# Kernel optimization log

Hardware: AMD Instinct MI355X
Metric: run time of the kernel (lower is better)

Reference implementation:

```python
import jax, jax.numpy as jnp
import numpy as np

TOP_K = 2
NUM_EXPERTS = 8

def setup_inputs() -> dict:
    key = jax.random.key(0)
    k_x, k_r, k_g, k_u, k_d = jax.random.split(key, 5)
    B, L, D, H, E = 1, 2048, 1024, 2048, NUM_EXPERTS
    scale = 0.02  # keep router logits / activations in a sane range
    return {
        "x": jax.random.normal(k_x, (B, L, D), dtype=jnp.float32),
        "router_w": jax.random.normal(k_r, (D, E), dtype=jnp.float32) * scale,
        "gate_w": jax.random.normal(k_g, (E, D, H), dtype=jnp.float32) * scale,
        "up_w": jax.random.normal(k_u, (E, D, H), dtype=jnp.float32) * scale,
        "down_w": jax.random.normal(k_d, (E, H, D), dtype=jnp.float32) * scale,
    }

def reference(x, router_w, gate_w, up_w, down_w):
    # x: (B, L, D)
    B, L, D = x.shape
    T = B * L
    E = router_w.shape[1]
    xf = x.reshape(T, D)

    # --- router: top-k softmax over selected logits (Mixtral-style) ---
    logits = xf @ router_w                      # (T, E)
    top_vals, top_idx = jax.lax.top_k(logits, TOP_K)  # (T, K)
    top_w = jax.nn.softmax(top_vals, axis=-1)   # (T, K)

    # combine weights scattered to dense (T, E); zeros for unrouted experts
    combine = jnp.zeros((T, E), dtype=x.dtype).at[
        jnp.arange(T)[:, None], top_idx
    ].add(top_w)

    # --- experts: SwiGLU, computed per expert, zero-weight tokens masked by combine ---
    gate = jnp.einsum('td,edh->eth', xf, gate_w)   # (E, T, H)
    up = jnp.einsum('td,edh->eth', xf, up_w)       # (E, T, H)
    hidden = jax.nn.silu(gate) * up                # (E, T, H)
    expert_out = jnp.einsum('eth,ehd->etd', hidden, down_w)  # (E, T, D)

    # --- weighted combine (equivalent to scatter_add over sorted assignments) ---
    y = jnp.einsum('etd,te->td', expert_out, combine)  # (T, D)
    return y.reshape(B, L, D)
```

## Files before the change

### kernel.cpp

```cpp
#include <hip/hip_runtime.h>
#include <hip/hip_bf16.h>
#include <stdint.h>

#define T_TOK 2048
#define DIM   1024
#define HDIM  2048
#define NE    8
#define ROWS_PAD 4224
#define TSLOTS 40

typedef __attribute__((ext_vector_type(8))) short bf16x8;
typedef __attribute__((ext_vector_type(8))) unsigned short u16x8;
typedef __attribute__((ext_vector_type(4))) float f32x4;

__device__ __forceinline__ unsigned short f2bf(float f) {
    union { float f; unsigned int u; } v; v.f = f;
    unsigned int r = v.u + 0x7FFF + ((v.u >> 16) & 1);
    return (unsigned short)(r >> 16);
}

__device__ __forceinline__ float bf2f(unsigned short b) {
    union { unsigned int u; float f; } v; v.u = ((unsigned int)b) << 16;
    return v.f;
}

__device__ __forceinline__ void gload16(const void* g, void* l) {
    __builtin_amdgcn_global_load_lds(
        (const __attribute__((address_space(1))) void*)g,
        (__attribute__((address_space(3))) void*)l, 16, 0, 0);
}

#define NTT 12288
__global__ void prep_kernel(const float* __restrict__ gw, const float* __restrict__ uw,
                            const float* __restrict__ dw,
                            unsigned short* __restrict__ WgT, unsigned short* __restrict__ WuT,
                            unsigned short* __restrict__ WdT,
                            const float* __restrict__ x, const float* __restrict__ rw,
                            int* __restrict__ counts, int* __restrict__ top_idx,
                            float* __restrict__ top_w) {
    __shared__ __align__(16) unsigned short lt[64 * 66];
    const int b = blockIdx.x;
    if (b < NTT) {
        const int m = b >> 12;
        const int t = b & 4095;
        const int e = t >> 9;
        const int rem = t & 511;
        const float* in; unsigned short* out; int R, C, by, bx;
        if (m == 0)      { in = gw; out = WgT; R = DIM;  C = HDIM; by = rem >> 5; bx = rem & 31; }
        else if (m == 1) { in = uw; out = WuT; R = DIM;  C = HDIM; by = rem >> 5; bx = rem & 31; }
        else             { in = dw; out = WdT; R = HDIM; C = DIM;  by = rem >> 4; bx = rem & 15; }
        const float* ip = in + (size_t)e * R * C + (size_t)(by * 64) * C + bx * 64;
        unsigned short* op = out + (size_t)e * R * C + (size_t)(bx * 64) * R + by * 64;
        const int r = threadIdx.x >> 2, g = threadIdx.x & 3;
#pragma unroll
        for (int i = 0; i < 4; ++i) {
            int s = g + 4 * i;
            float4 v = *(const float4*)&ip[(size_t)r * C + s * 4];
            ushort4 h;
            h.x = f2bf(v.x); h.y = f2bf(v.y); h.z = f2bf(v.z); h.w = f2bf(v.w);
            *(ushort4*)&lt[r * 66 + s * 4] = h;
        }
        __syncthreads();
        const int oc = threadIdx.x >> 2;
#pragma unroll
        for (int i = 0; i < 2; ++i) {
            int s = g + 4 * i;
            u16x8 h;
#pragma unroll
            for (int k = 0; k < 8; ++k)
                h[k] = lt[(s * 8 + k) * 66 + oc];
            *(u16x8*)&op[(size_t)oc * R + s * 8] = h;
        }
    } else {
        const int wid = (b - NTT) * 4 + (threadIdx.x >> 6);
        const int lane = threadIdx.x & 63;
        if (wid >= T_TOK) return;
        float acc[NE];
#pragma unroll
        for (int e = 0; e < NE; ++e) acc[e] = 0.f;
        const float* xr = x + (size_t)wid * DIM;
        for (int i = lane; i < DIM; i += 64) {
            float xv = xr[i];
            const float* wr = rw + (size_t)i * NE;
#pragma unroll
            for (int e = 0; e < NE; ++e) acc[e] += xv * wr[e];
        }
#pragma unroll
        for (int off = 32; off; off >>= 1) {
#pragma unroll
            for (int e = 0; e < NE; ++e) acc[e] += __shfl_xor(acc[e], off, 64);
        }
        if (lane == 0) {
            float v0 = -1e30f, v1 = -1e30f; int i0 = 0, i1 = 0;
#pragma unroll
            for (int e = 0; e < NE; ++e) {
                float v = acc[e];
                if (v > v0) { v1 = v0; i1 = i0; v0 = v; i0 = e; }
                else if (v > v1) { v1 = v; i1 = e; }
            }
            float e1 = __expf(v1 - v0);
            float s = 1.f + e1;
            top_idx[wid * 2]     = i0;
            top_idx[wid * 2 + 1] = i1;
            top_w[wid * 2]     = 1.f / s;
            top_w[wid * 2 + 1] = e1 / s;
            atomicAdd(&counts[i0], 1);
            atomicAdd(&counts[i1], 1);
        }
    }
}

__global__ void scan_kernel(const int* __restrict__ counts, int* __restrict__ offsets,
                            int* __restrict__ cursors,
                            int* __restrict__ tl_e, int* __restrict__ tl_m) {
    if (threadIdx.x == 0) {
        int run = 0;
        for (int e = 0; e < NE; ++e) { offsets[e] = run; cursors[e] = run; run += counts[e]; }
        int n = 0;
        for (int e = 0; e < NE; ++e) {
            int mt = (counts[e] + 127) >> 7;
            for (int m = 0; m < mt && n < 64; ++m) { tl_e[n] = e; tl_m[n] = m; ++n; }
        }
        for (; n < 64; ++n) tl_e[n] = -1;
    }
}

__global__ void gather_kernel(const float* __restrict__ x, const int* __restrict__ top_idx,
                              const float* __restrict__ top_w, int* __restrict__ cursors,
                              int* __restrict__ row_tok, float* __restrict__ row_w,
                              unsigned short* __restrict__ Abuf) {
    int t = blockIdx.x;
    __shared__ int pos[2];
    if (threadIdx.x < 2) {
        int k = threadIdx.x;
        int e = top_idx[t * 2 + k];
        int p = atomicAdd(&cursors[e], 1);
        pos[k] = p;
        row_tok[p] = t;
        row_w[p] = top_w[t * 2 + k];
    }
    __syncthreads();
    const float4* xr = (const float4*)(x + (size_t)t * DIM);
    float4 v = xr[threadIdx.x];
    ushort4 b;
    b.x = f2bf(v.x); b.y = f2bf(v.y); b.z = f2bf(v.z); b.w = f2bf(v.w);
    ushort4* A4 = (ushort4*)Abuf;
    A4[(size_t)pos[0] * (DIM / 4) + threadIdx.x] = b;
    A4[(size_t)pos[1] * (DIM / 4) + threadIdx.x] = b;
}

__global__ __launch_bounds__(256, 2)
void gemm1_kernel(const unsigned short* __restrict__ Abuf,
                  const unsigned short* __restrict__ WgT,
                  const unsigned short* __restrict__ WuT,
                  unsigned short* __restrict__ Hbuf,
                  const int* __restrict__ offsets, const int* __restrict__ counts,
                  const int* __restrict__ tl_e, const int* __restrict__ tl_m) {
    const int slot = blockIdx.y;
    const int e = tl_e[slot];
    if (e < 0) return;
    const int mtile = tl_m[slot];
    const int cnt = counts[e];
    const int n0 = blockIdx.x * 64;
    const int row0 = offsets[e] + mtile * 128;

    __shared__ __align__(16) unsigned char lds_raw[65536];
    unsigned short* AsB = (unsigned short*)lds_raw;
    unsigned short* BgB = (unsigned short*)(lds_raw + 32768);
    unsigned short* BuB = (unsigned short*)(lds_raw + 49152);
    unsigned short* ex  = (unsigned short*)lds_raw;

    const int tid = threadIdx.x;
    const int lane = tid & 63;
    const int wave = tid >> 6;
    const int wm = wave >> 1;
    const int wu = wave & 1;

    f32x4 acc[4][4];
#pragma unroll
    for (int i = 0; i < 4; ++i)
#pragma unroll
        for (int j = 0; j < 4; ++j) acc[i][j] = (f32x4){0.f, 0.f, 0.f, 0.f};

    const int srow = tid >> 3;
    const int sc0 = tid & 7;
    const unsigned short* Aab = Abuf + (size_t)row0 * DIM;
    const unsigned short* Bgb = WgT + (size_t)e * HDIM * DIM + (size_t)n0 * DIM;
    const unsigned short* Bub = WuT + (size_t)e * HDIM * DIM + (size_t)n0 * DIM;

    auto stage = [&](int buf, int kt) {
#pragma unroll
        for (int i = 0; i < 4; ++i) {
            int row = i * 32 + srow;
            int csrc = sc0 ^ (row & 7);
            gload16(Aab + (size_t)row * DIM + kt + csrc * 8,
                    AsB + buf * 8192 + (i * 256 + tid) * 8);
        }
#pragma unroll
        for (int i = 0; i < 2; ++i) {
            int row = i * 32 + srow;
            int csrc = sc0 ^ (row & 7);
            size_t go = (size_t)row * DIM + kt + csrc * 8;
            gload16(Bgb + go, BgB + buf * 4096 + (i * 256 + tid) * 8);
            gload16(Bub + go, BuB + buf * 4096 + (i * 256 + tid) * 8);
        }
    };

    const int rsel = lane & 15;
    const int csrcf = lane >> 4;

    stage(0, 0);
    int cur = 0;
    for (int kt = 0; kt < DIM; kt += 64) {
        __syncthreads();
        if (kt + 64 < DIM) stage(cur ^ 1, kt + 64);
        const unsigned short* Ac = AsB + cur * 8192;
        const unsigned short* Bc = (wu ? BuB : BgB) + cur * 4096;
#pragma unroll
        for (int kk = 0; kk < 2; ++kk) {
            bf16x8 af[4], bb[4];
#pragma unroll
            for (int i = 0; i < 4; ++i) {
                int ra = wm * 64 + i * 16 + rsel;
                af[i] = *(const bf16x8*)&Ac[ra * 64 + ((kk * 4 + csrcf) ^ (ra & 7)) * 8];
                int rb = i * 16 + rsel;
                bb[i] = *(const bf16x8*)&Bc[rb * 64 + ((kk * 4 + csrcf) ^ (rb & 7)) * 8];
            }
#pragma unroll
            for (int i = 0; i < 4; ++i)
#pragma unroll
                for (int j = 0; j < 4; ++j)
                    acc[i][j] = __builtin_amdgcn_mfma_f32_16x16x32_bf16(af[i], bb[j], acc[i][j], 0, 0, 0);
        }
        cur ^= 1;
    }

    const int c = lane & 15, rbase = (lane >> 4) * 4;
    const int obase = offsets[e];
    __syncthreads();
    if (wu) {
#pragma unroll
        for (int i = 0; i < 4; ++i)
#pragma unroll
            for (int r = 0; r < 4; ++r) {
                int row64 = i * 16 + rbase + r;
#pragma unroll
                for (int j = 0; j < 4; ++j)
                    ex[wm * 4096 + row64 * 64 + j * 16 + c] = f2bf(acc[i][j][r]);
            }
    }
    __syncthreads();
    if (!wu) {
#pragma unroll
        for (int i = 0; i < 4; ++i) {
#pragma unroll
            for (int r = 0; r < 4; ++r) {
                int row64 = i * 16 + rbase + r;
                int lrow = mtile * 128 + wm * 64 + row64;
                if (lrow < cnt) {
                    size_t orow = (size_t)(obase + lrow);
#pragma unroll
                    for (int j = 0; j < 4; ++j) {
                        float g = acc[i][j][r];
                        float u = bf2f(ex[wm * 4096 + row64 * 64 + j * 16 + c]);
                        float h = g * u / (1.f + __expf(-g));
                        Hbuf[orow * HDIM + n0 + j * 16 + c] = f2bf(h);
                    }
                }
            }
        }
    }
}

__global__ __launch_bounds__(256, 2)
void gemm2_kernel(const unsigned short* __restrict__ Hbuf,
                  const unsigned short* __restrict__ WdT,
                  float* __restrict__ y,
                  const int* __restrict__ offsets, const int* __restrict__ counts,
                  const int* __restrict__ row_tok, const float* __restrict__ row_w,
                  const int* __restrict__ tl_e, const int* __restrict__ tl_m) {
    const int slot = blockIdx.y;
    const int e = tl_e[slot];
    if (e < 0) return;
    const int mtile = tl_m[slot];
    const int kc = blockIdx.z;
    const int cnt = counts[e];
    const int n0 = blockIdx.x * 128;
    const int row0 = offsets[e] + mtile * 128;

    __shared__ unsigned short As[2][128 * 64];
    __shared__ unsigned short Bs[2][128 * 64];

    const int tid = threadIdx.x;
    const int lane = tid & 63;
    const int wave = tid >> 6;
    const int wm = wave >> 1, wn = wave & 1;

    f32x4 acc[4][4];
#pragma unroll
    for (int i = 0; i < 4; ++i)
#pragma unroll
        for (int j = 0; j < 4; ++j) acc[i][j] = (f32x4){0.f, 0.f, 0.f, 0.f};

    const int srow0 = tid >> 3;
    const int sc0 = tid & 7;
    const unsigned short* Aab = Hbuf + (size_t)row0 * HDIM;
    const unsigned short* Bbb = WdT + (size_t)e * DIM * HDIM + (size_t)n0 * HDIM;

    auto stage = [&](int buf, int kt) {
#pragma unroll
        for (int i = 0; i < 4; ++i) {
            int row = i * 32 + srow0;
            int csrc = sc0 ^ (row & 7);
            size_t go = (size_t)row * HDIM + kt + csrc * 8;
            int lo = (i * 256 + tid) * 8;
            gload16(Aab + go, &As[buf][lo]);
            gload16(Bbb + go, &Bs[buf][lo]);
        }
    };

    const int rsel = lane & 15;
    const int csrcf = lane >> 4;

    const int kbeg = kc * (HDIM / 2);
    const int kend = kbeg + (HDIM / 2);

    stage(0, kbeg);
    int cur = 0;
    for (int kt = kbeg; kt < kend; kt += 64) {
        __syncthreads();
        if (kt + 64 < kend) stage(cur ^ 1, kt + 64);
        const unsigned short* Ac = As[cur];
        const unsigned short* Bc = Bs[cur];
#pragma unroll
        for (int kk = 0; kk < 2; ++kk) {
            bf16x8 af[4], bf[4];
#pragma unroll
            for (int i = 0; i < 4; ++i) {
                int ra = wm * 64 + i * 16 + rsel;
                af[i] = *(const bf16x8*)&Ac[ra * 64 + ((kk * 4 + csrcf) ^ (ra & 7)) * 8];
                int rb = wn * 64 + i * 16 + rsel;
                bf[i] = *(const bf16x8*)&Bc[rb * 64 + ((kk * 4 + csrcf) ^ (rb & 7)) * 8];
            }
#pragma unroll
            for (int i = 0; i < 4; ++i)
#pragma unroll
                for (int j = 0; j < 4; ++j)
                    acc[i][j] = __builtin_amdgcn_mfma_f32_16x16x32_bf16(af[i], bf[j], acc[i][j], 0, 0, 0);
        }
        cur ^= 1;
    }

    const int c = lane & 15, rbase = (lane >> 4) * 4;
    const int obase = offsets[e];
#pragma unroll
    for (int i = 0; i < 4; ++i) {
#pragma unroll
        for (int r = 0; r < 4; ++r) {
            int lrow = mtile * 128 + wm * 64 + i * 16 + rbase + r;
            if (lrow < cnt) {
                int grow = obase + lrow;
                int tok = row_tok[grow];
                float w = row_w[grow];
#pragma unroll
                for (int j = 0; j < 4; ++j) {
                    atomicAdd(&y[(size_t)tok * DIM + n0 + wn * 64 + j * 16 + c], w * acc[i][j][r]);
                }
            }
        }
    }
}

extern "C" void kernel_launch(void* const* d_in, const int* in_sizes, int n_in,
                              void* d_out, int out_size, void* d_ws, size_t ws_size,
                              hipStream_t stream) {
    const float* x  = (const float*)d_in[0];
    const float* rw = (const float*)d_in[1];
    const float* gw = (const float*)d_in[2];
    const float* uw = (const float*)d_in[3];
    const float* dw = (const float*)d_in[4];
    float* y = (float*)d_out;

    char* ws = (char*)d_ws;
    int*   counts  = (int*)(ws + 0);
    int*   cursors = (int*)(ws + 32);
    int*   offsets = (int*)(ws + 64);
    int*   top_idx = (int*)(ws + 128);
    float* top_w   = (float*)(ws + 128 + 16384);
    int*   row_tok = (int*)(ws + 128 + 32768);
    float* row_w   = (float*)(ws + 128 + 32768 + 16896);
    int*   tl_e    = (int*)(ws + 128 + 32768 + 2 * 16896);
    int*   tl_m    = (int*)(ws + 128 + 32768 + 2 * 16896 + 256);
    size_t off = 128 + 32768 + 2 * 16896 + 512;
    off = (off + 255) & ~(size_t)255;
    unsigned short* Abuf = (unsigned short*)(ws + off); off += (size_t)ROWS_PAD * DIM * 2;
    unsigned short* Hbuf = (unsigned short*)(ws + off); off += (size_t)ROWS_PAD * HDIM * 2;
    unsigned short* WgT  = (unsigned short*)(ws + off); off += (size_t)NE * DIM * HDIM * 2;
    unsigned short* WuT  = (unsigned short*)(ws + off); off += (size_t)NE * DIM * HDIM * 2;
    unsigned short* WdT  = (unsigned short*)(ws + off); off += (size_t)NE * DIM * HDIM * 2;
    if (ws_size < off) return;

    hipMemsetAsync(counts, 0, 32, stream);
    hipMemsetAsync(d_out, 0, (size_t)out_size * 4, stream);

    prep_kernel<<<NTT + T_TOK / 4, 256, 0, stream>>>(gw, uw, dw, WgT, WuT, WdT,
                                                     x, rw, counts, top_idx, top_w);
    scan_kernel<<<1, 64, 0, stream>>>(counts, offsets, cursors, tl_e, tl_m);
    gather_kernel<<<T_TOK, 256, 0, stream>>>(x, top_idx, top_w, cursors, row_tok, row_w, Abuf);

    gemm1_kernel<<<dim3(HDIM / 64, TSLOTS), 256, 0, stream>>>(Abuf, WgT, WuT, Hbuf,
                                                              offsets, counts, tl_e, tl_m);
    gemm2_kernel<<<dim3(DIM / 128, TSLOTS, 2), 256, 0, stream>>>(Hbuf, WdT, y, offsets, counts,
                                                                 row_tok, row_w, tl_e, tl_m);
}
```

Baseline: 257.3 us.

## Enlarge weight transpose tiles to 512x64 with batched loads per block

The fp32-to-bf16 weight transpose in the prep kernel now handles a 512x64 tile per block instead of 64x64, which cuts the number of blocks eightfold. Each thread issues eight float4 loads before converting, to keep more memory requests in flight, and each output row is written as a contiguous 1 KB segment by a full wave. The cost is a much larger LDS tile (about 68 KB) and a launch bound of two blocks per CU, which may limit occupancy. The host launch grid presumably has to match the new NTT.

```diff
diff --git a/kernel.cpp b/kernel.cpp
--- a/kernel.cpp
+++ b/kernel.cpp
@@ -30,46 +30,52 @@
         (__attribute__((address_space(3))) void*)l, 16, 0, 0);
 }
 
-#define NTT 12288
-__global__ void prep_kernel(const float* __restrict__ gw, const float* __restrict__ uw,
-                            const float* __restrict__ dw,
-                            unsigned short* __restrict__ WgT, unsigned short* __restrict__ WuT,
-                            unsigned short* __restrict__ WdT,
-                            const float* __restrict__ x, const float* __restrict__ rw,
-                            int* __restrict__ counts, int* __restrict__ top_idx,
-                            float* __restrict__ top_w) {
-    __shared__ __align__(16) unsigned short lt[64 * 66];
+#define NTT 1536
+__global__ __launch_bounds__(256, 2)
+void prep_kernel(const float* __restrict__ gw, const float* __restrict__ uw,
+                 const float* __restrict__ dw,
+                 unsigned short* __restrict__ WgT, unsigned short* __restrict__ WuT,
+                 unsigned short* __restrict__ WdT,
+                 const float* __restrict__ x, const float* __restrict__ rw,
+                 int* __restrict__ counts, int* __restrict__ top_idx,
+                 float* __restrict__ top_w) {
+    __shared__ __align__(16) unsigned short lt[512][68];
     const int b = blockIdx.x;
     if (b < NTT) {
-        const int m = b >> 12;
-        const int t = b & 4095;
-        const int e = t >> 9;
-        const int rem = t & 511;
-        const float* in; unsigned short* out; int R, C, by, bx;
-        if (m == 0)      { in = gw; out = WgT; R = DIM;  C = HDIM; by = rem >> 5; bx = rem & 31; }
-        else if (m == 1) { in = uw; out = WuT; R = DIM;  C = HDIM; by = rem >> 5; bx = rem & 31; }
-        else             { in = dw; out = WdT; R = HDIM; C = DIM;  by = rem >> 4; bx = rem & 15; }
-        const float* ip = in + (size_t)e * R * C + (size_t)(by * 64) * C + bx * 64;
-        unsigned short* op = out + (size_t)e * R * C + (size_t)(bx * 64) * R + by * 64;
-        const int r = threadIdx.x >> 2, g = threadIdx.x & 3;
-#pragma unroll
-        for (int i = 0; i < 4; ++i) {
-            int s = g + 4 * i;
-            float4 v = *(const float4*)&ip[(size_t)r * C + s * 4];
-            ushort4 h;
-            h.x = f2bf(v.x); h.y = f2bf(v.y); h.z = f2bf(v.z); h.w = f2bf(v.w);
-            *(ushort4*)&lt[r * 66 + s * 4] = h;
+        const int m = b >> 9;
+        const int t = b & 511;
+        const int e = t >> 6;
+        const int rem = t & 63;
+        const float* in; unsigned short* out; int Ri, Ci, ri, ci;
+        if (m == 0)      { in = gw; out = WgT; Ri = DIM;  Ci = HDIM; ri = rem & 1; ci = rem >> 1; }
+        else if (m == 1) { in = uw; out = WuT; Ri = DIM;  Ci = HDIM; ri = rem & 1; ci = rem >> 1; }
+        else             { in = dw; out = WdT; Ri = HDIM; Ci = DIM;  ri = rem & 3; ci = rem >> 2; }
+        const float* ip = in + (size_t)e * Ri * Ci + (size_t)(ri * 512) * Ci + ci * 64;
+        unsigned short* op = out + (size_t)e * Ri * Ci + (size_t)(ci * 64) * Ri + ri * 512;
+        const int s = threadIdx.x & 15;
+        const int rb = threadIdx.x >> 4;
+#pragma unroll
+        for (int ii = 0; ii < 4; ++ii) {
+            float4 v[8];
+#pragma unroll
+            for (int j = 0; j < 8; ++j)
+                v[j] = *(const float4*)&ip[(size_t)(rb + 16 * (ii * 8 + j)) * Ci + s * 4];
+#pragma unroll
+            for (int j = 0; j < 8; ++j) {
+                ushort4 h;
+                h.x = f2bf(v[j].x); h.y = f2bf(v[j].y); h.z = f2bf(v[j].z); h.w = f2bf(v[j].w);
+                *(ushort4*)&lt[rb + 16 * (ii * 8 + j)][s * 4] = h;
+            }
         }
         __syncthreads();
-        const int oc = threadIdx.x >> 2;
-#pragma unroll
-        for (int i = 0; i < 2; ++i) {
-            int s = g + 4 * i;
+        const int w = threadIdx.x >> 6, l = threadIdx.x & 63;
+#pragma unroll
+        for (int i = 0; i < 16; ++i) {
+            int c = w + 4 * i;
             u16x8 h;
 #pragma unroll
-            for (int k = 0; k < 8; ++k)
-                h[k] = lt[(s * 8 + k) * 66 + oc];
-            *(u16x8*)&op[(size_t)oc * R + s * 8] = h;
+            for (int k = 0; k < 8; ++k) h[k] = lt[l * 8 + k][c];
+            *(u16x8*)&op[(size_t)c * Ri + l * 8] = h;
         }
     } else {
         const int wid = (b - NTT) * 4 + (threadIdx.x >> 6);
```

Result: slower. 278.4 us (+8.2%).
